# Optimization experiments

Hardware: AMD Instinct MI355X
Metric: run time of the kernel (lower is better)

The kernel has to match this reference:

```python
import jax, jax.numpy as jnp
import numpy as np

NEG_BIG = -9.0e15

def setup_inputs() -> dict:
    key = jax.random.key(0)
    k1, k2, k3, k4 = jax.random.split(key, 4)
    N, F_in, F_out = 2048, 512, 64
    x = jax.random.normal(k1, (N, F_in), dtype=jnp.float32)
    adj = jax.random.randint(k2, (N, N), 0, 2, dtype=jnp.int32)
    # xavier_uniform with gain=1.414
    def xavier(k, shape, gain=1.414):
        fan_in, fan_out = shape[0], shape[1]
        bound = gain * np.sqrt(6.0 / (fan_in + fan_out))
        return jax.random.uniform(k, shape, jnp.float32, -bound, bound)
    W = xavier(k3, (F_in, F_out))
    a = xavier(k4, (F_out, 1))
    return {"x": x, "adj": adj, "W": W, "a": a}

def reference(x, adj, W, a):
    h = x @ W                                  # [N, F_out]
    # pairwise |h_i - h_j| projected by a: e[i,j] = relu(sum_f |h_i,f - h_j,f| * a_f)
    diff = jnp.abs(h[:, None, :] - h[None, :, :])   # [N, N, F_out]
    e = jax.nn.relu(jnp.einsum('ijf,fo->ij', diff, a))  # [N, N]
    scores = jnp.where(adj > 0, e, NEG_BIG)
    attention = jax.nn.softmax(scores, axis=1)
    out = attention @ h                        # [N, F_out]
    return jax.nn.relu(out)                    # concat=True path
```

## Files before the change

### kernel.cpp

```cpp
#include <hip/hip_runtime.h>

#define Nn 2048
#define FIN 512
#define FO 64
#define SHIFT 20.0f
#define NJT 32
#define JR (Nn / NJT)
#define HS 68
#define PTS 68
#define ZTOT (Nn * FO + Nn)

#define HX(r, f) ((r) * HS + ((((f) >> 2) ^ (((r) >> 2) & 15)) << 2))

__global__ __launch_bounds__(256) void gat_xw(const float* __restrict__ x,
                                              const float* __restrict__ W,
                                              float* __restrict__ h,
                                              float* __restrict__ z) {
    const int gt = blockIdx.x * 256 + threadIdx.x;
    if (z != nullptr && gt < ZTOT) z[gt] = 0.f;

    __shared__ float part[2][2][FO];
    const int wave = threadIdx.x >> 6;
    const int lane = threadIdx.x & 63;
    const int rs = wave >> 1;
    const int kh = wave & 1;
    int row = blockIdx.x * 2 + rs;
    row = __builtin_amdgcn_readfirstlane(row);
    const float* xr = x + (size_t)row * FIN + kh * (FIN / 2);
    const float* Wp = W + (size_t)kh * (FIN / 2) * FO;
    float acc = 0.f;
#pragma unroll 2
    for (int k = 0; k < FIN / 2; k += 8) {
        float4 xa = *(const float4*)(xr + k);
        float4 xb = *(const float4*)(xr + k + 4);
        acc = fmaf(xa.x, Wp[(k + 0) * FO + lane], acc);
        acc = fmaf(xa.y, Wp[(k + 1) * FO + lane], acc);
        acc = fmaf(xa.z, Wp[(k + 2) * FO + lane], acc);
        acc = fmaf(xa.w, Wp[(k + 3) * FO + lane], acc);
        acc = fmaf(xb.x, Wp[(k + 4) * FO + lane], acc);
        acc = fmaf(xb.y, Wp[(k + 5) * FO + lane], acc);
        acc = fmaf(xb.z, Wp[(k + 6) * FO + lane], acc);
        acc = fmaf(xb.w, Wp[(k + 7) * FO + lane], acc);
    }
    part[rs][kh][lane] = acc;
    __syncthreads();
    if (threadIdx.x < 128) {
        const int r2 = threadIdx.x >> 6;
        const int l2 = threadIdx.x & 63;
        h[((size_t)blockIdx.x * 2 + r2) * FO + l2] = part[r2][0][l2] + part[r2][1][l2];
    }
}

template <bool ATOMIC>
__global__ __launch_bounds__(256, 4) void gat_attn(const float* __restrict__ h,
                                                   const int* __restrict__ adj,
                                                   const float* __restrict__ a,
                                                   float* __restrict__ po,
                                                   float* __restrict__ pl) {
    __shared__ __align__(16) float up[64 * PTS];
    __shared__ __align__(16) float hj_s[64 * HS];
    __shared__ __align__(16) float a_s[FO];
    float* hi_s = up;
    float* pT_s = up;

    const int tid = threadIdx.x;
    const int w = tid >> 6;
    const int lane = tid & 63;
    const int li = lane & 3;
    const int lj = lane >> 2;
    const int it = blockIdx.x >> 5;
    const int jt = blockIdx.x & (NJT - 1);
    const int ib = it * 64;
    const int jb = jt * JR;
    const int iw = w * 16;

    for (int g4 = tid; g4 < 1024; g4 += 256) {
        const int row = g4 >> 4;
        const int f0 = (g4 & 15) * 4;
        float4 v = *(const float4*)(h + (size_t)ib * FO + (size_t)g4 * 4);
        *(float4*)&hi_s[HX(row, f0)] = v;
        float4 u = *(const float4*)(h + (size_t)jb * FO + (size_t)g4 * 4);
        *(float4*)&hj_s[HX(row, f0)] = u;
    }
    if (tid < FO) a_s[tid] = a[tid];
    __syncthreads();

    int4 am[4];
#pragma unroll
    for (int di = 0; di < 4; di++)
        am[di] = *(const int4*)(adj + (size_t)(ib + iw + 4 * li + di) * Nn + (jb + 4 * lj));

    float pv[4][4];
    float ls[4];
#pragma unroll
    for (int u = 0; u < 4; u++) {
        ls[u] = 0.f;
#pragma unroll
        for (int v2 = 0; v2 < 4; v2++) pv[u][v2] = 0.f;
    }

    float e[4][4];
#pragma unroll
    for (int di = 0; di < 4; di++)
#pragma unroll
        for (int dj = 0; dj < 4; dj++) e[di][dj] = 0.f;

#pragma unroll 4
    for (int f = 0; f < FO; f += 4) {
        const float4 av = *(const float4*)&a_s[f];
        float4 hi4[4], hj4[4];
#pragma unroll
        for (int d = 0; d < 4; d++) {
            hi4[d] = *(const float4*)&hi_s[HX(iw + 4 * li + d, f)];
            hj4[d] = *(const float4*)&hj_s[HX(4 * lj + d, f)];
        }
#pragma unroll
        for (int di = 0; di < 4; di++)
#pragma unroll
            for (int dj = 0; dj < 4; dj++) {
                e[di][dj] = fmaf(fabsf(hi4[di].x - hj4[dj].x), av.x, e[di][dj]);
                e[di][dj] = fmaf(fabsf(hi4[di].y - hj4[dj].y), av.y, e[di][dj]);
                e[di][dj] = fmaf(fabsf(hi4[di].z - hj4[dj].z), av.z, e[di][dj]);
                e[di][dj] = fmaf(fabsf(hi4[di].w - hj4[dj].w), av.w, e[di][dj]);
            }
    }

#pragma unroll
    for (int di = 0; di < 4; di++) {
        const int* ap = (const int*)&am[di];
#pragma unroll
        for (int dj = 0; dj < 4; dj++) {
            const float p = (ap[dj] > 0) ? __expf(fmaxf(e[di][dj], 0.f) - SHIFT) : 0.f;
            e[di][dj] = p;
            ls[di] += p;
        }
    }

    __syncthreads();

#pragma unroll
    for (int dj = 0; dj < 4; dj++) {
        *(float4*)&pT_s[(4 * lj + dj) * PTS + iw + 4 * li] =
            make_float4(e[0][dj], e[1][dj], e[2][dj], e[3][dj]);
    }
    __syncthreads();

#pragma unroll 4
    for (int j = 0; j < 64; j++) {
        const float4 pj = *(const float4*)&pT_s[j * PTS + iw + 4 * li];
        const float4 hv = *(const float4*)&hj_s[HX(j, 4 * lj)];
        pv[0][0] = fmaf(pj.x, hv.x, pv[0][0]);
        pv[0][1] = fmaf(pj.x, hv.y, pv[0][1]);
        pv[0][2] = fmaf(pj.x, hv.z, pv[0][2]);
        pv[0][3] = fmaf(pj.x, hv.w, pv[0][3]);
        pv[1][0] = fmaf(pj.y, hv.x, pv[1][0]);
        pv[1][1] = fmaf(pj.y, hv.y, pv[1][1]);
        pv[1][2] = fmaf(pj.y, hv.z, pv[1][2]);
        pv[1][3] = fmaf(pj.y, hv.w, pv[1][3]);
        pv[2][0] = fmaf(pj.z, hv.x, pv[2][0]);
        pv[2][1] = fmaf(pj.z, hv.y, pv[2][1]);
        pv[2][2] = fmaf(pj.z, hv.z, pv[2][2]);
        pv[2][3] = fmaf(pj.z, hv.w, pv[2][3]);
        pv[3][0] = fmaf(pj.w, hv.x, pv[3][0]);
        pv[3][1] = fmaf(pj.w, hv.y, pv[3][1]);
        pv[3][2] = fmaf(pj.w, hv.z, pv[3][2]);
        pv[3][3] = fmaf(pj.w, hv.w, pv[3][3]);
    }

#pragma unroll
    for (int di = 0; di < 4; di++) {
        float v = ls[di];
        v += __shfl_xor(v, 4, 64);
        v += __shfl_xor(v, 8, 64);
        v += __shfl_xor(v, 16, 64);
        v += __shfl_xor(v, 32, 64);
        ls[di] = v;
    }

    if constexpr (!ATOMIC) {
        if (lj == 0) {
#pragma unroll
            for (int di = 0; di < 4; di++)
                pl[(size_t)jt * Nn + (ib + iw + 4 * li + di)] = ls[di];
        }
#pragma unroll
        for (int di = 0; di < 4; di++)
            *(float4*)&po[((size_t)jt * Nn + (ib + iw + 4 * li + di)) * FO + 4 * lj] =
                make_float4(pv[di][0], pv[di][1], pv[di][2], pv[di][3]);
    } else {
        if (lj == 0) {
#pragma unroll
            for (int di = 0; di < 4; di++)
                atomicAdd(&pl[ib + iw + 4 * li + di], ls[di]);
        }
#pragma unroll
        for (int di = 0; di < 4; di++) {
#pragma unroll
            for (int v2 = 0; v2 < 4; v2++)
                atomicAdd(&po[(size_t)(ib + iw + 4 * li + di) * FO + 4 * lj + v2], pv[di][v2]);
        }
    }
}

__global__ __launch_bounds__(256) void gat_reduce(const float* __restrict__ po,
                                                  const float* __restrict__ pl,
                                                  float* __restrict__ out) {
    const int t = blockIdx.x * 256 + threadIdx.x;
    const int i = t >> 6;
    float s = 0.f;
#pragma unroll
    for (int p = 0; p < NJT; p++) s += po[(size_t)p * (Nn * FO) + t];
    float l = 0.f;
#pragma unroll
    for (int p = 0; p < NJT; p++) l += pl[p * Nn + i];
    out[t] = fmaxf(s / l, 0.f);
}

__global__ __launch_bounds__(256) void gat_fin(const float* __restrict__ osum,
                                               const float* __restrict__ lsum,
                                               float* __restrict__ out) {
    const int t = blockIdx.x * 256 + threadIdx.x;
    out[t] = fmaxf(osum[t] / lsum[t >> 6], 0.f);
}

extern "C" void kernel_launch(void* const* d_in, const int* in_sizes, int n_in,
                              void* d_out, int out_size, void* d_ws, size_t ws_size,
                              hipStream_t stream) {
    const float* x   = (const float*)d_in[0];
    const int*   adj = (const int*)d_in[1];
    const float* W   = (const float*)d_in[2];
    const float* a   = (const float*)d_in[3];
    float* out = (float*)d_out;

    float* h = (float*)d_ws;
    const size_t need = ((size_t)Nn * FO + (size_t)NJT * Nn * FO + (size_t)NJT * Nn) * 4;

    if (ws_size >= need) {
        float* po = h + (size_t)Nn * FO;
        float* pl = po + (size_t)NJT * Nn * FO;
        gat_xw<<<dim3(1024), dim3(256), 0, stream>>>(x, W, h, nullptr);
        gat_attn<false><<<dim3(32 * NJT), dim3(256), 0, stream>>>(h, adj, a, po, pl);
        gat_reduce<<<dim3(512), dim3(256), 0, stream>>>(po, pl, out);
    } else {
        float* osum = h + (size_t)Nn * FO;
        float* lsum = osum + (size_t)Nn * FO;
        gat_xw<<<dim3(1024), dim3(256), 0, stream>>>(x, W, h, osum);
        gat_attn<true><<<dim3(32 * NJT), dim3(256), 0, stream>>>(h, adj, a, osum, lsum);
        gat_fin<<<dim3(512), dim3(256), 0, stream>>>(osum, lsum, out);
    }
}
```

Before: 118.4 us.

## Read h directly from global/L1 in attention kernel instead of LDS tiles

Replaces the attention kernel's shared-memory staging of the h_i and h_j tiles with direct global loads. Each lane now owns one i row and 16 j columns, and the h_j rows are read through the cache, where they are broadcast across lanes. Only the probability tile stays in per-wave LDS, so the block-wide __syncthreads barriers go away. The aim is to cut LDS traffic, LDS footprint and synchronisation, at the cost of relying on L1/L2 hit rates and lower register-level reuse of h.

```diff
diff --git a/kernel.cpp b/kernel.cpp
--- a/kernel.cpp
+++ b/kernel.cpp
@@ -5,12 +5,8 @@
 #define FO 64
 #define SHIFT 20.0f
 #define NJT 32
-#define JR (Nn / NJT)
-#define HS 68
-#define PTS 68
+#define PS 68
 #define ZTOT (Nn * FO + Nn)
-
-#define HX(r, f) ((r) * HS + ((((f) >> 2) ^ (((r) >> 2) & 15)) << 2))
 
 __global__ __launch_bounds__(256) void gat_xw(const float* __restrict__ x,
                                               const float* __restrict__ W,
@@ -52,153 +48,110 @@
 }
 
 template <bool ATOMIC>
-__global__ __launch_bounds__(256, 4) void gat_attn(const float* __restrict__ h,
-                                                   const int* __restrict__ adj,
-                                                   const float* __restrict__ a,
-                                                   float* __restrict__ po,
-                                                   float* __restrict__ pl) {
-    __shared__ __align__(16) float up[64 * PTS];
-    __shared__ __align__(16) float hj_s[64 * HS];
-    __shared__ __align__(16) float a_s[FO];
-    float* hi_s = up;
-    float* pT_s = up;
+__global__ __launch_bounds__(256, 4) void gat_attn5(const float* __restrict__ h,
+                                                    const int* __restrict__ adj,
+                                                    const float* __restrict__ a,
+                                                    float* __restrict__ po,
+                                                    float* __restrict__ pl) {
+    __shared__ __align__(16) float p_s[4][16 * PS];
 
     const int tid = threadIdx.x;
     const int w = tid >> 6;
     const int lane = tid & 63;
-    const int li = lane & 3;
-    const int lj = lane >> 2;
+    const int il = lane & 15;
+    const int g = lane >> 4;
     const int it = blockIdx.x >> 5;
     const int jt = blockIdx.x & (NJT - 1);
     const int ib = it * 64;
-    const int jb = jt * JR;
-    const int iw = w * 16;
-
-    for (int g4 = tid; g4 < 1024; g4 += 256) {
-        const int row = g4 >> 4;
-        const int f0 = (g4 & 15) * 4;
-        float4 v = *(const float4*)(h + (size_t)ib * FO + (size_t)g4 * 4);
-        *(float4*)&hi_s[HX(row, f0)] = v;
-        float4 u = *(const float4*)(h + (size_t)jb * FO + (size_t)g4 * 4);
-        *(float4*)&hj_s[HX(row, f0)] = u;
-    }
-    if (tid < FO) a_s[tid] = a[tid];
-    __syncthreads();
-
-    int4 am[4];
-#pragma unroll
-    for (int di = 0; di < 4; di++)
-        am[di] = *(const int4*)(adj + (size_t)(ib + iw + 4 * li + di) * Nn + (jb + 4 * lj));
-
-    float pv[4][4];
-    float ls[4];
-#pragma unroll
-    for (int u = 0; u < 4; u++) {
-        ls[u] = 0.f;
-#pragma unroll
-        for (int v2 = 0; v2 < 4; v2++) pv[u][v2] = 0.f;
-    }
+    const int jb = jt * 64;
+    const int i = ib + w * 16 + il;
+    const int jB = jb + g * 16;
+
+    const float* hrow = h + (size_t)i * FO;
 
     float e[4][4];
 #pragma unroll
-    for (int di = 0; di < 4; di++)
-#pragma unroll
-        for (int dj = 0; dj < 4; dj++) e[di][dj] = 0.f;
-
-#pragma unroll 4
-    for (int f = 0; f < FO; f += 4) {
-        const float4 av = *(const float4*)&a_s[f];
-        float4 hi4[4], hj4[4];
-#pragma unroll
-        for (int d = 0; d < 4; d++) {
-            hi4[d] = *(const float4*)&hi_s[HX(iw + 4 * li + d, f)];
-            hj4[d] = *(const float4*)&hj_s[HX(4 * lj + d, f)];
+    for (int q = 0; q < 4; q++)
+#pragma unroll
+        for (int k = 0; k < 4; k++) e[q][k] = 0.f;
+
+#pragma unroll 2
+    for (int f4 = 0; f4 < 16; f4++) {
+        const float4 av = *(const float4*)(a + f4 * 4);
+        const float4 hi = *(const float4*)(hrow + f4 * 4);
+#pragma unroll
+        for (int q = 0; q < 4; q++) {
+#pragma unroll
+            for (int k = 0; k < 4; k++) {
+                const float4 hj = *(const float4*)(h + (size_t)(jB + q * 4 + k) * FO + f4 * 4);
+                e[q][k] = fmaf(fabsf(hi.x - hj.x), av.x, e[q][k]);
+                e[q][k] = fmaf(fabsf(hi.y - hj.y), av.y, e[q][k]);
+                e[q][k] = fmaf(fabsf(hi.z - hj.z), av.z, e[q][k]);
+                e[q][k] = fmaf(fabsf(hi.w - hj.w), av.w, e[q][k]);
+            }
         }
-#pragma unroll
-        for (int di = 0; di < 4; di++)
-#pragma unroll
-            for (int dj = 0; dj < 4; dj++) {
-                e[di][dj] = fmaf(fabsf(hi4[di].x - hj4[dj].x), av.x, e[di][dj]);
-                e[di][dj] = fmaf(fabsf(hi4[di].y - hj4[dj].y), av.y, e[di][dj]);
-                e[di][dj] = fmaf(fabsf(hi4[di].z - hj4[dj].z), av.z, e[di][dj]);
-                e[di][dj] = fmaf(fabsf(hi4[di].w - hj4[dj].w), av.w, e[di][dj]);
-            }
-    }
-
-#pragma unroll
-    for (int di = 0; di < 4; di++) {
-        const int* ap = (const int*)&am[di];
-#pragma unroll
-        for (int dj = 0; dj < 4; dj++) {
-            const float p = (ap[dj] > 0) ? __expf(fmaxf(e[di][dj], 0.f) - SHIFT) : 0.f;
-            e[di][dj] = p;
-            ls[di] += p;
+    }
+
+    float ls = 0.f;
+#pragma unroll
+    for (int q = 0; q < 4; q++) {
+        const int4 am = *(const int4*)(adj + (size_t)i * Nn + jB + q * 4);
+        float4 pq;
+        pq.x = (am.x > 0) ? __expf(fmaxf(e[q][0], 0.f) - SHIFT) : 0.f;
+        pq.y = (am.y > 0) ? __expf(fmaxf(e[q][1], 0.f) - SHIFT) : 0.f;
+        pq.z = (am.z > 0) ? __expf(fmaxf(e[q][2], 0.f) - SHIFT) : 0.f;
+        pq.w = (am.w > 0) ? __expf(fmaxf(e[q][3], 0.f) - SHIFT) : 0.f;
+        ls += pq.x + pq.y + pq.z + pq.w;
+        *(float4*)&p_s[w][il * PS + g * 16 + q * 4] = pq;
+    }
+
+    const int fo = g * 16;
+    float4 o0 = make_float4(0.f, 0.f, 0.f, 0.f);
+    float4 o1 = o0, o2 = o0, o3 = o0;
+#pragma unroll 2
+    for (int j4 = 0; j4 < 16; j4++) {
+        const float4 p4 = *(const float4*)&p_s[w][il * PS + j4 * 4];
+#pragma unroll
+        for (int k = 0; k < 4; k++) {
+            const float pk = (k == 0) ? p4.x : (k == 1) ? p4.y : (k == 2) ? p4.z : p4.w;
+            const float* hj = h + (size_t)(jb + j4 * 4 + k) * FO + fo;
+            const float4 h0 = *(const float4*)(hj);
+            const float4 h1 = *(const float4*)(hj + 4);
+            const float4 h2 = *(const float4*)(hj + 8);
+            const float4 h3 = *(const float4*)(hj + 12);
+            o0.x = fmaf(pk, h0.x, o0.x); o0.y = fmaf(pk, h0.y, o0.y);
+            o0.z = fmaf(pk, h0.z, o0.z); o0.w = fmaf(pk, h0.w, o0.w);
+            o1.x = fmaf(pk, h1.x, o1.x); o1.y = fmaf(pk, h1.y, o1.y);
+            o1.z = fmaf(pk, h1.z, o1.z); o1.w = fmaf(pk, h1.w, o1.w);
+            o2.x = fmaf(pk, h2.x, o2.x); o2.y = fmaf(pk, h2.y, o2.y);
+            o2.z = fmaf(pk, h2.z, o2.z); o2.w = fmaf(pk, h2.w, o2.w);
+            o3.x = fmaf(pk, h3.x, o3.x); o3.y = fmaf(pk, h3.y, o3.y);
+            o3.z = fmaf(pk, h3.z, o3.z); o3.w = fmaf(pk, h3.w, o3.w);
         }
     }
 
-    __syncthreads();
-
-#pragma unroll
-    for (int dj = 0; dj < 4; dj++) {
-        *(float4*)&pT_s[(4 * lj + dj) * PTS + iw + 4 * li] =
-            make_float4(e[0][dj], e[1][dj], e[2][dj], e[3][dj]);
-    }
-    __syncthreads();
-
-#pragma unroll 4
-    for (int j = 0; j < 64; j++) {
-        const float4 pj = *(const float4*)&pT_s[j * PTS + iw + 4 * li];
-        const float4 hv = *(const float4*)&hj_s[HX(j, 4 * lj)];
-        pv[0][0] = fmaf(pj.x, hv.x, pv[0][0]);
-        pv[0][1] = fmaf(pj.x, hv.y, pv[0][1]);
-        pv[0][2] = fmaf(pj.x, hv.z, pv[0][2]);
-        pv[0][3] = fmaf(pj.x, hv.w, pv[0][3]);
-        pv[1][0] = fmaf(pj.y, hv.x, pv[1][0]);
-        pv[1][1] = fmaf(pj.y, hv.y, pv[1][1]);
-        pv[1][2] = fmaf(pj.y, hv.z, pv[1][2]);
-        pv[1][3] = fmaf(pj.y, hv.w, pv[1][3]);
-        pv[2][0] = fmaf(pj.z, hv.x, pv[2][0]);
-        pv[2][1] = fmaf(pj.z, hv.y, pv[2][1]);
-        pv[2][2] = fmaf(pj.z, hv.z, pv[2][2]);
-        pv[2][3] = fmaf(pj.z, hv.w, pv[2][3]);
-        pv[3][0] = fmaf(pj.w, hv.x, pv[3][0]);
-        pv[3][1] = fmaf(pj.w, hv.y, pv[3][1]);
-        pv[3][2] = fmaf(pj.w, hv.z, pv[3][2]);
-        pv[3][3] = fmaf(pj.w, hv.w, pv[3][3]);
-    }
-
-#pragma unroll
-    for (int di = 0; di < 4; di++) {
-        float v = ls[di];
-        v += __shfl_xor(v, 4, 64);
-        v += __shfl_xor(v, 8, 64);
-        v += __shfl_xor(v, 16, 64);
-        v += __shfl_xor(v, 32, 64);
-        ls[di] = v;
-    }
+    float lv = ls;
+    lv += __shfl_xor(lv, 16, 64);
+    lv += __shfl_xor(lv, 32, 64);
 
     if constexpr (!ATOMIC) {
-        if (lj == 0) {
-#pragma unroll
-            for (int di = 0; di < 4; di++)
-                pl[(size_t)jt * Nn + (ib + iw + 4 * li + di)] = ls[di];
-        }
-#pragma unroll
-        for (int di = 0; di < 4; di++)
-            *(float4*)&po[((size_t)jt * Nn + (ib + iw + 4 * li + di)) * FO + 4 * lj] =
-                make_float4(pv[di][0], pv[di][1], pv[di][2], pv[di][3]);
+        if (lane < 16) pl[(size_t)jt * Nn + i] = lv;
+        float* dst = po + ((size_t)jt * Nn + i) * FO + fo;
+        *(float4*)(dst)      = o0;
+        *(float4*)(dst + 4)  = o1;
+        *(float4*)(dst + 8)  = o2;
+        *(float4*)(dst + 12) = o3;
     } else {
-        if (lj == 0) {
-#pragma unroll
-            for (int di = 0; di < 4; di++)
-                atomicAdd(&pl[ib + iw + 4 * li + di], ls[di]);
-        }
-#pragma unroll
-        for (int di = 0; di < 4; di++) {
-#pragma unroll
-            for (int v2 = 0; v2 < 4; v2++)
-                atomicAdd(&po[(size_t)(ib + iw + 4 * li + di) * FO + 4 * lj + v2], pv[di][v2]);
-        }
+        if (lane < 16) atomicAdd(&pl[i], lv);
+        float* dst = po + (size_t)i * FO + fo;
+        atomicAdd(dst + 0,  o0.x); atomicAdd(dst + 1,  o0.y);
+        atomicAdd(dst + 2,  o0.z); atomicAdd(dst + 3,  o0.w);
+        atomicAdd(dst + 4,  o1.x); atomicAdd(dst + 5,  o1.y);
+        atomicAdd(dst + 6,  o1.z); atomicAdd(dst + 7,  o1.w);
+        atomicAdd(dst + 8,  o2.x); atomicAdd(dst + 9,  o2.y);
+        atomicAdd(dst + 10, o2.z); atomicAdd(dst + 11, o2.w);
+        atomicAdd(dst + 12, o3.x); atomicAdd(dst + 13, o3.y);
+        atomicAdd(dst + 14, o3.z); atomicAdd(dst + 15, o3.w);
     }
 }
 
@@ -239,13 +192,13 @@
         float* po = h + (size_t)Nn * FO;
         float* pl = po + (size_t)NJT * Nn * FO;
         gat_xw<<<dim3(1024), dim3(256), 0, stream>>>(x, W, h, nullptr);
-        gat_attn<false><<<dim3(32 * NJT), dim3(256), 0, stream>>>(h, adj, a, po, pl);
+        gat_attn5<false><<<dim3(32 * NJT), dim3(256), 0, stream>>>(h, adj, a, po, pl);
         gat_reduce<<<dim3(512), dim3(256), 0, stream>>>(po, pl, out);
     } else {
         float* osum = h + (size_t)Nn * FO;
         float* lsum = osum + (size_t)Nn * FO;
         gat_xw<<<dim3(1024), dim3(256), 0, stream>>>(x, W, h, osum);
-        gat_attn<true><<<dim3(32 * NJT), dim3(256), 0, stream>>>(h, adj, a, osum, lsum);
+        gat_attn5<true><<<dim3(32 * NJT), dim3(256), 0, stream>>>(h, adj, a, osum, lsum);
         gat_fin<<<dim3(512), dim3(256), 0, stream>>>(osum, lsum, out);
     }
 }
```

New measurement: 160.5 us. 35.6% more time.
